# Optimization experiments

Hardware: AMD Instinct MI355X
Metric: run time of the kernel (lower is better)

## Reference

```python
import jax, jax.numpy as jnp
import numpy as np

N = 200000      # total nodes
E = 800000      # directed edges
G = 4096        # graphs in batch
D_DRUG = 128
D_CELL = 954
HID = 128
OUT = 128
EPS = 1e-5      # BatchNorm eps


def _bn(x, gamma, beta):
    # training-mode BatchNorm1d (batch statistics, biased var), dropout is eval/identity
    m = jnp.mean(x, axis=0)
    v = jnp.mean((x - m) ** 2, axis=0)
    return gamma * (x - m) * jax.lax.rsqrt(v + EPS) + beta


def _gcn_conv(x, edge_index, W, b):
    # PyG GCNConv: add self-loops, symmetric normalization, aggregate, then bias
    src = jnp.concatenate([edge_index[0], jnp.arange(N)])
    dst = jnp.concatenate([edge_index[1], jnp.arange(N)])
    ones = jnp.ones(src.shape[0], dtype=x.dtype)
    deg = jax.ops.segment_sum(ones, dst, num_segments=N)
    dinv = jnp.where(deg > 0, jax.lax.rsqrt(jnp.maximum(deg, 1.0)), 0.0)
    norm = dinv[src] * dinv[dst]                      # [E+N]
    h = x @ W                                         # [N, out]
    msg = h[src] * norm[:, None]                      # gather + scale
    out = jax.ops.segment_sum(msg, dst, num_segments=N)  # scatter-add
    return out + b


def setup_inputs() -> dict:
    key = jax.random.key(0)
    ks = jax.random.split(key, 12)
    x = jax.random.normal(ks[0], (N, D_DRUG), jnp.float32)
    edge_index = jax.random.randint(ks[1], (2, E), 0, N)
    ibatch = (jnp.arange(N) * G) // N  # sorted, every graph non-empty
    gexpr = jax.random.normal(ks[2], (G, D_CELL), jnp.float32)

    def w(k, shape):
        return jax.random.normal(k, shape, jnp.float32) / np.float32(np.sqrt(shape[0]))

    return {
        "x": x, "edge_index": edge_index, "ibatch": ibatch, "gexpr": gexpr,
        "W1": w(ks[3], (D_DRUG, HID)), "b1": jnp.zeros((HID,), jnp.float32),
        "g1": jnp.ones((HID,), jnp.float32), "be1": jnp.zeros((HID,), jnp.float32),
        "W2": w(ks[4], (HID, OUT)), "b2": jnp.zeros((OUT,), jnp.float32),
        "g2": jnp.ones((OUT,), jnp.float32), "be2": jnp.zeros((OUT,), jnp.float32),
        "Wc1": w(ks[5], (D_CELL, HID)), "bc1": jnp.zeros((HID,), jnp.float32),
        "gc": jnp.ones((HID,), jnp.float32), "bec": jnp.zeros((HID,), jnp.float32),
        "Wc2": w(ks[6], (HID, OUT)), "bc2": jnp.zeros((OUT,), jnp.float32),
    }


def reference(x, edge_index, ibatch, gexpr,
              W1, b1, g1, be1, W2, b2, g2, be2,
              Wc1, bc1, gc, bec, Wc2, bc2):
    # drug branch
    h = _gcn_conv(x, edge_index, W1, b1)
    h = _bn(jax.nn.relu(h), g1, be1)
    h = _gcn_conv(h, edge_index, W2, b2)
    h = _bn(jax.nn.relu(h), g2, be2)
    x_drug = jax.ops.segment_max(h, ibatch, num_segments=G)  # global_max_pool
    # cellline branch
    c = jnp.tanh(gexpr @ Wc1 + bc1)
    c = _bn(c, gc, bec)
    x_cell = jax.nn.relu(c @ Wc2 + bc2)
    return x_drug, x_cell
```

## Files before the change

### kernel.cpp

```cpp
#include <hip/hip_runtime.h>

#define NFEAT 128

typedef __attribute__((ext_vector_type(4))) float f32x4;
typedef __attribute__((ext_vector_type(8))) short bf16x8;

__device__ __forceinline__ unsigned short f2bf(float f) {
    unsigned u = __builtin_bit_cast(unsigned, f);
    u += 0x7fffu + ((u >> 16) & 1u);
    return (unsigned short)(u >> 16);
}
__device__ __forceinline__ float bf2f(unsigned short s) {
    unsigned u = ((unsigned)s) << 16;
    return __builtin_bit_cast(float, u);
}

__device__ __forceinline__ void dma16(const void* g, void* l) {
    __builtin_amdgcn_global_load_lds(
        (const __attribute__((address_space(1))) unsigned int*)g,
        (__attribute__((address_space(3))) unsigned int*)l, 16, 0, 0);
}

template <int ACT, typename OutT>
__device__ __forceinline__ void gemm_loop(
    int tfirst, int tstride, int tcount, int by,
    const unsigned short* __restrict__ A, const unsigned short* __restrict__ Bt,
    OutT* __restrict__ C, int M, int ldA, int ldB,
    const float* __restrict__ bias, const float* __restrict__ dscale, char* smem)
{
    unsigned short* buf0 = (unsigned short*)smem;
    unsigned short* buf1 = buf0 + 64 * 128;
    const int tid = threadIdx.x;
    const int wv = tid >> 6, lane = tid & 63;
    const int l16 = lane & 15, quad = lane >> 4;
    const int kbase = by * 128;

    const int nc0 = (wv & 1) * 64;
    bf16x8 bfr[4][4];
#pragma unroll
    for (int nt = 0; nt < 4; ++nt) {
        const unsigned short* bp =
            Bt + (size_t)(nc0 + nt * 16 + l16) * ldB + kbase + quad * 8;
#pragma unroll
        for (int ks = 0; ks < 4; ++ks)
            bfr[nt][ks] = *(const bf16x8*)(bp + ks * 32);
    }

    C += (size_t)by * M * NFEAT;
    const int rh = wv >> 1;
    const int r0 = wv * 16;

    auto stage = [&](unsigned short* dst, long tile) {
        const long t0 = tile * 64;
#pragma unroll
        for (int j = 0; j < 4; ++j) {
            const unsigned short* gp = A +
                (size_t)(t0 + r0 + j * 4 + (lane >> 4)) * ldA + kbase + l16 * 8;
            dma16(gp, (void*)&dst[(r0 + j * 4) * 128]);
        }
    };

    if (tfirst < tcount) stage(buf0, tfirst);
    __syncthreads();

    int cur = 0;
    for (long t = tfirst; t < tcount; t += tstride) {
        unsigned short* bufc = cur ? buf1 : buf0;
        unsigned short* bufn = cur ? buf0 : buf1;
        const long tn = t + tstride;
        if (tn < tcount) stage(bufn, tn);

        bf16x8 af[2][4];
#pragma unroll
        for (int mt = 0; mt < 2; ++mt) {
            const int row = rh * 32 + mt * 16 + l16;
#pragma unroll
            for (int ks = 0; ks < 4; ++ks)
                af[mt][ks] = *(const bf16x8*)(bufc + row * 128 + ks * 32 + quad * 8);
        }

        f32x4 acc[2][4];
#pragma unroll
        for (int a = 0; a < 2; ++a)
#pragma unroll
            for (int b = 0; b < 4; ++b) acc[a][b] = (f32x4){0.f, 0.f, 0.f, 0.f};
#pragma unroll
        for (int ks = 0; ks < 4; ++ks)
#pragma unroll
            for (int nt = 0; nt < 4; ++nt)
#pragma unroll
                for (int mt = 0; mt < 2; ++mt)
                    acc[mt][nt] = __builtin_amdgcn_mfma_f32_16x16x32_bf16(
                        af[mt][ks], bfr[nt][ks], acc[mt][nt], 0, 0, 0);

        const long tile0 = t * 64;
        float ds[2][4];
#pragma unroll
        for (int mt = 0; mt < 2; ++mt)
#pragma unroll
            for (int r = 0; r < 4; ++r) {
                long row = tile0 + rh * 32 + mt * 16 + quad * 4 + r;
                ds[mt][r] = dscale ? dscale[row] : 1.f;
            }
#pragma unroll
        for (int nt = 0; nt < 4; ++nt) {
            int col = nc0 + nt * 16 + l16;
            float bv = bias ? bias[col] : 0.f;
#pragma unroll
            for (int mt = 0; mt < 2; ++mt) {
                long rbase = tile0 + rh * 32 + mt * 16 + quad * 4;
#pragma unroll
                for (int r = 0; r < 4; ++r) {
                    float v = acc[mt][nt][r] + bv;
                    if (ACT == 1) v = tanhf(v);
                    if (ACT == 2) v = fmaxf(v, 0.f);
                    v *= ds[mt][r];
                    if constexpr (sizeof(OutT) == 2)
                        C[(size_t)(rbase + r) * NFEAT + col] = (OutT)f2bf(v);
                    else
                        C[(size_t)(rbase + r) * NFEAT + col] = (OutT)v;
                }
            }
        }
        __syncthreads();
        cur ^= 1;
    }
}

__global__ void k_prep(const float* __restrict__ W1, unsigned short* __restrict__ W1t,
                       const float* __restrict__ Wc1, unsigned short* __restrict__ Wc1t,
                       const float* __restrict__ gexpr, unsigned short* __restrict__ Apadh,
                       const int* __restrict__ dst, int* __restrict__ deg,
                       int G, int DC, int DCP, int E, int r1, int r2, int r3)
{
    int b = blockIdx.x, t = threadIdx.x;
    if (b < r1) {
        int idx = b * 256 + t;
        int n = idx >> 7, k = idx & 127;
        W1t[idx] = f2bf(W1[(size_t)k * NFEAT + n]);
    } else if (b < r2) {
        int idx = (b - r1) * 256 + t;
        int n = idx >> 10, k = idx & 1023;
        Wc1t[idx] = (k < DC) ? f2bf(Wc1[(size_t)k * NFEAT + n]) : (unsigned short)0;
    } else if (b < r3) {
        long idx = (long)(b - r2) * 256 + t;
        if (idx < (long)G * DCP) {
            long i = idx / DCP; int k = (int)(idx - i * DCP);
            Apadh[idx] = (k < DC) ? f2bf(gexpr[i * DC + k]) : (unsigned short)0;
        }
    } else {
        int e = (b - r3) * 256 + t;
        if (e < E) atomicAdd(&deg[dst[e]], 1);
    }
}

__device__ __forceinline__ void bnfold_body(
    int bb, const float* __restrict__ sums8, const float* __restrict__ gamma,
    const float* __restrict__ beta, float invN,
    const float* __restrict__ W, const float* __restrict__ extra,
    unsigned short* __restrict__ Wt, float* __restrict__ brow)
{
    __shared__ float ssc[128], ssh[128];
    int t = threadIdx.x;
    if (t < 128) {
        float s = 0.f, s2 = 0.f;
#pragma unroll
        for (int c = 0; c < 8; ++c) { s += sums8[c * 256 + t]; s2 += sums8[c * 256 + 128 + t]; }
        float mean = s * invN;
        float var = s2 * invN - mean * mean;
        float rstd = rsqrtf(fmaxf(var, 0.f) + 1e-5f);
        float sc = gamma[t] * rstd;
        ssc[t] = sc;
        ssh[t] = beta[t] - mean * sc;
    }
    __syncthreads();
    if (bb < 64) {
        int idx = bb * 256 + t;
        int n = idx >> 7, k = idx & 127;
        Wt[idx] = f2bf(W[(size_t)k * NFEAT + n] * ssc[k]);
    } else if (t < 128) {
        float s = extra ? extra[t] : 0.f;
        for (int k = 0; k < 128; ++k) s += ssh[k] * W[(size_t)k * NFEAT + t];
        brow[t] = s;
    }
}

__global__ void k_bnfold2(
    const float* sA, const float* gA, const float* bA, float invA,
    const float* WA, const float* eA, unsigned short* WtA, float* browA,
    const float* sB, const float* gB, const float* bB, float invB,
    const float* WB, const float* eB, unsigned short* WtB, float* browB)
{
    int b = blockIdx.x;
    if (b < 65) bnfold_body(b, sA, gA, bA, invA, WA, eA, WtA, browA);
    else        bnfold_body(b - 65, sB, gB, bB, invB, WB, eB, WtB, browB);
}

__global__ __launch_bounds__(256) void k_scan1(const int* __restrict__ deg,
        int* __restrict__ rowptr, int* __restrict__ bsum, float* __restrict__ dinv, int N)
{
    __shared__ int sh[256];
    int t = threadIdx.x;
    int base = blockIdx.x * 1024 + t * 4;
    int v[4];
#pragma unroll
    for (int j = 0; j < 4; ++j) {
        v[j] = (base + j < N) ? deg[base + j] : 0;
        if (base + j < N) dinv[base + j] = rsqrtf((float)(v[j] + 1));
    }
    int s = v[0] + v[1] + v[2] + v[3];
    sh[t] = s;
    __syncthreads();
    int incl = s;
    for (int off = 1; off < 256; off <<= 1) {
        int x = (t >= off) ? sh[t - off] : 0;
        __syncthreads();
        incl += x;
        sh[t] = incl;
        __syncthreads();
    }
    int run = incl - s;
#pragma unroll
    for (int j = 0; j < 4; ++j) {
        if (base + j < N) rowptr[base + j] = run;
        run += v[j];
    }
    if (t == 255) bsum[blockIdx.x] = incl;
}

__global__ void k_scan2(int* __restrict__ bsum, int nb)
{
    __shared__ int sh[256];
    int t = threadIdx.x;
    int s = (t < nb) ? bsum[t] : 0;
    sh[t] = s;
    __syncthreads();
    int incl = s;
    for (int off = 1; off < 256; off <<= 1) {
        int x = (t >= off) ? sh[t - off] : 0;
        __syncthreads();
        incl += x;
        sh[t] = incl;
        __syncthreads();
    }
    if (t < nb) bsum[t] = incl - s;
}

__global__ void k_scan3(int* __restrict__ rowptr, int* __restrict__ cursor,
                        const int* __restrict__ bsum, int N, int E)
{
    int i = blockIdx.x * 256 + threadIdx.x;
    if (i < N) {
        int v = rowptr[i] + bsum[i >> 10];
        rowptr[i] = v;
        cursor[i] = v;
    } else if (i == N) {
        rowptr[N] = E;
    }
}

__global__ void k_fillconv(const int* __restrict__ src, const int* __restrict__ dst,
                           int* __restrict__ cursor, int* __restrict__ csr, int E, int nf,
                           const float* __restrict__ x, unsigned short* __restrict__ xb,
                           long nfloat)
{
    const int b = blockIdx.x;
    int role, idx;
    if (b < 2 * nf) { role = b & 1; idx = b >> 1; }
    else            { role = 0;     idx = b - nf; }

    if (role == 1) {
        int e = idx * 256 + threadIdx.x;
        if (e < E) {
            int pos = atomicAdd(&cursor[dst[e]], 1);
            csr[pos] = src[e];
        }
    } else {
        long base = (long)idx * 4096 + (long)threadIdx.x * 16;
        if (base < nfloat) {
            f32x4 v0 = *(const f32x4*)(x + base);
            f32x4 v1 = *(const f32x4*)(x + base + 4);
            f32x4 v2 = *(const f32x4*)(x + base + 8);
            f32x4 v3 = *(const f32x4*)(x + base + 12);
            unsigned short o[16];
#pragma unroll
            for (int j = 0; j < 4; ++j) {
                o[j] = f2bf(v0[j]); o[4 + j] = f2bf(v1[j]);
                o[8 + j] = f2bf(v2[j]); o[12 + j] = f2bf(v3[j]);
            }
            *(uint4*)(xb + base) = *(const uint4*)&o[0];
            *(uint4*)(xb + base + 8) = *(const uint4*)&o[8];
        }
    }
}

__global__ __launch_bounds__(256) void k_pair1(
    const unsigned short* __restrict__ xb, const unsigned short* __restrict__ W1t,
    unsigned short* __restrict__ h, int N, const float* __restrict__ dinv,
    const unsigned short* __restrict__ Apadh, const unsigned short* __restrict__ Wc1t,
    float* __restrict__ pbuf, int G, int nb1, int gtiles)
{
    extern __shared__ char smem[];
    int b = blockIdx.x;
    if (b < nb1) {
        gemm_loop<0, unsigned short>(b, nb1, gtiles, 0,
                                     xb, W1t, h, N, 128, 128,
                                     nullptr, dinv, smem);
    } else {
        int cb = b - nb1;
        gemm_loop<0, float>(cb & 15, 16, 64, cb >> 4,
                            Apadh, Wc1t, pbuf, G, 1024, 1024,
                            nullptr, nullptr, smem);
    }
}

__device__ __forceinline__ void unpack_add(float* acc, uint4 a)
{
    acc[0] += bf2f((unsigned short)(a.x & 0xffff));
    acc[1] += bf2f((unsigned short)(a.x >> 16));
    acc[2] += bf2f((unsigned short)(a.y & 0xffff));
    acc[3] += bf2f((unsigned short)(a.y >> 16));
    acc[4] += bf2f((unsigned short)(a.z & 0xffff));
    acc[5] += bf2f((unsigned short)(a.z >> 16));
    acc[6] += bf2f((unsigned short)(a.w & 0xffff));
    acc[7] += bf2f((unsigned short)(a.w >> 16));
}

__device__ __forceinline__ void row_gather(const unsigned short* __restrict__ h,
    const int* __restrict__ rowptr, const int* __restrict__ csr,
    long i, int f, float* acc)
{
    int lo = rowptr[i], hi = rowptr[i + 1];
    int e = lo;
    for (; e + 3 < hi; e += 4) {
        int s0 = csr[e], s1 = csr[e + 1], s2 = csr[e + 2], s3 = csr[e + 3];
        uint4 a = *(const uint4*)(h + ((size_t)s0 << 7) + f);
        uint4 b = *(const uint4*)(h + ((size_t)s1 << 7) + f);
        uint4 c = *(const uint4*)(h + ((size_t)s2 << 7) + f);
        uint4 d = *(const uint4*)(h + ((size_t)s3 << 7) + f);
        unpack_add(acc, a); unpack_add(acc, b);
        unpack_add(acc, c); unpack_add(acc, d);
    }
    for (; e < hi; ++e) {
        int s0 = csr[e];
        uint4 a = *(const uint4*)(h + ((size_t)s0 << 7) + f);
        unpack_add(acc, a);
    }
    uint4 hs = *(const uint4*)(h + ((size_t)i << 7) + f);
    unpack_add(acc, hs);
}

__global__ __launch_bounds__(256) void k_pair2(
    const unsigned short* __restrict__ h, const int* __restrict__ rowptr,
    const int* __restrict__ csr, const float* __restrict__ dinv,
    const float* __restrict__ bias, unsigned short* __restrict__ out,
    float* __restrict__ sums8, int N, int na,
    const float* __restrict__ p, const float* __restrict__ biasC,
    unsigned short* __restrict__ cbuf, float* __restrict__ sumsC, int G)
{
    __shared__ float red[4][256];
    const int tid = threadIdx.x;
    if (blockIdx.x >= na) {
        int bb = blockIdx.x - na;
        int j = tid & 127;
        int slot = bb * 2 + (tid >> 7);
        const int nslots = 64;
        const size_t st = (size_t)G * NFEAT;
        float b = biasC[j], s = 0.f, s2 = 0.f;
        for (int i = slot; i < G; i += nslots) {
            size_t o = (size_t)i * NFEAT + j;
            float v = b;
#pragma unroll
            for (int c = 0; c < 8; ++c) v += p[o + c * st];
            v = tanhf(v);
            cbuf[o] = f2bf(v);
            s += v; s2 += v * v;
        }
        atomicAdd(&sumsC[(bb & 7) * 256 + j], s);
        atomicAdd(&sumsC[(bb & 7) * 256 + 128 + j], s2);
        return;
    }
    const int wv = tid >> 6, lane = tid & 63;
    const int f = (tid & 15) << 3;
    const long g0 = (long)blockIdx.x * 16 + (tid >> 4);
    const long gstride = (long)na * 16;

    f32x4 b0 = *(const f32x4*)&bias[f];
    f32x4 b1 = *(const f32x4*)&bias[f + 4];

    float s8[8], q8[8];
#pragma unroll
    for (int j = 0; j < 8; ++j) { s8[j] = 0.f; q8[j] = 0.f; }

    for (long i = g0; i < N; i += gstride) {
        float acc[8];
#pragma unroll
        for (int j = 0; j < 8; ++j) acc[j] = 0.f;
        row_gather(h, rowptr, csr, i, f, acc);

        float di = dinv[i];
        unsigned short o[8];
#pragma unroll
        for (int j = 0; j < 8; ++j) {
            float bj = (j < 4) ? b0[j] : b1[j - 4];
            float v = fmaxf(di * acc[j] + bj, 0.f);
            o[j] = f2bf(v);
            s8[j] += v; q8[j] += v * v;
        }
        *(uint4*)(out + (i << 7) + f) = *(const uint4*)o;
    }

#pragma unroll
    for (int j = 0; j < 8; ++j) {
        s8[j] += __shfl_xor(s8[j], 16);
        s8[j] += __shfl_xor(s8[j], 32);
        q8[j] += __shfl_xor(q8[j], 16);
        q8[j] += __shfl_xor(q8[j], 32);
    }
    if (lane < 16) {
#pragma unroll
        for (int j = 0; j < 8; ++j) {
            red[wv][f + j] = s8[j];
            red[wv][128 + f + j] = q8[j];
        }
    }
    __syncthreads();
    float tot = red[0][tid] + red[1][tid] + red[2][tid] + red[3][tid];
    atomicAdd(&sums8[(blockIdx.x & 7) * 256 + tid], tot);
}

__global__ __launch_bounds__(256) void k_pair4(
    const unsigned short* __restrict__ agg, const unsigned short* __restrict__ W2t,
    unsigned short* __restrict__ h, int N, const float* __restrict__ brow2,
    const float* __restrict__ dinv,
    const unsigned short* __restrict__ cbuf, const unsigned short* __restrict__ Wc2t,
    float* __restrict__ outc, int G, const float* __restrict__ browC,
    int nb2, int gtiles)
{
    extern __shared__ char smem[];
    int b = blockIdx.x;
    if (b < nb2) {
        gemm_loop<0, unsigned short>(b, nb2, gtiles, 0,
                                     agg, W2t, h, N, 128, 128,
                                     brow2, dinv, smem);
    } else {
        gemm_loop<2, float>(b - nb2, 64, 64, 0,
                            cbuf, Wc2t, outc, G, 128, 128,
                            browC, nullptr, smem);
    }
}

__global__ __launch_bounds__(256) void k_aggmax(
    const unsigned short* __restrict__ h, const int* __restrict__ rowptr,
    const int* __restrict__ csr, const float* __restrict__ dinv,
    const float* __restrict__ bias, int* __restrict__ gmax, int* __restrict__ gmin,
    float* __restrict__ sums8, int N, int G)
{
    __shared__ float red[4][256];
    __shared__ int lmax[288], lmin[288];
    const int tid = threadIdx.x;
    const int wv = tid >> 6, lane = tid & 63;
    const int f8 = tid & 15;
    const int f = f8 << 3;
    const int grp = tid >> 4;
    const int g_lo = blockIdx.x * 2;
    const int rstart = (int)(((long long)g_lo * N + G - 1) / G);
    const int rend   = (int)(((long long)(g_lo + 2) * N + G - 1) / G);
    const int bnd1   = (int)(((long long)(g_lo + 1) * N + G - 1) / G);

    for (int idx = tid; idx < 288; idx += 256) {
        lmax[idx] = 0;
        lmin[idx] = 0x7f800000;
    }
    __syncthreads();

    f32x4 b0 = *(const f32x4*)&bias[f];
    f32x4 b1 = *(const f32x4*)&bias[f + 4];

    float s8[8], q8[8], rmx[8], rmn[8];
#pragma unroll
    for (int j = 0; j < 8; ++j) {
        s8[j] = 0.f; q8[j] = 0.f;
        rmx[j] = 0.f; rmn[j] = __builtin_bit_cast(float, 0x7f800000);
    }
    int cur = 0;

    for (long i = rstart + grp; i < rend; i += 16) {
        float acc[8];
#pragma unroll
        for (int j = 0; j < 8; ++j) acc[j] = 0.f;
        row_gather(h, rowptr, csr, i, f, acc);

        float di = dinv[i];
        int gi = (i >= bnd1);
        if (gi != cur) {
#pragma unroll
            for (int j = 0; j < 8; ++j) {
                atomicMax(&lmax[cur * 144 + j * 16 + f8], __builtin_bit_cast(int, rmx[j]));
                atomicMin(&lmin[cur * 144 + j * 16 + f8], __builtin_bit_cast(int, rmn[j]));
                rmx[j] = 0.f; rmn[j] = __builtin_bit_cast(float, 0x7f800000);
            }
            cur = gi;
        }
#pragma unroll
        for (int j = 0; j < 8; ++j) {
            float bj = (j < 4) ? b0[j] : b1[j - 4];
            float v = fmaxf(di * acc[j] + bj, 0.f);
            s8[j] += v; q8[j] += v * v;
            rmx[j] = fmaxf(rmx[j], v);
            rmn[j] = fminf(rmn[j], v);
        }
    }
#pragma unroll
    for (int j = 0; j < 8; ++j) {
        atomicMax(&lmax[cur * 144 + j * 16 + f8], __builtin_bit_cast(int, rmx[j]));
        atomicMin(&lmin[cur * 144 + j * 16 + f8], __builtin_bit_cast(int, rmn[j]));
    }

#pragma unroll
    for (int j = 0; j < 8; ++j) {
        s8[j] += __shfl_xor(s8[j], 16);
        s8[j] += __shfl_xor(s8[j], 32);
        q8[j] += __shfl_xor(q8[j], 16);
        q8[j] += __shfl_xor(q8[j], 32);
    }
    if (lane < 16) {
#pragma unroll
        for (int j = 0; j < 8; ++j) {
            red[wv][f + j] = s8[j];
            red[wv][128 + f + j] = q8[j];
        }
    }
    __syncthreads();
    float tot = red[0][tid] + red[1][tid] + red[2][tid] + red[3][tid];
    atomicAdd(&sums8[(blockIdx.x & 7) * 256 + tid], tot);

    for (int idx = tid; idx < 2 * 128; idx += 256) {
        int gg = idx >> 7, feat = idx & 127;
        int a = gg * 144 + (feat & 7) * 16 + (feat >> 3);
        gmax[(size_t)(g_lo + gg) * 128 + feat] = lmax[a];
        gmin[(size_t)(g_lo + gg) * 128 + feat] = lmin[a];
    }
}

__global__ void k_segfin(const float* __restrict__ sums8, const float* __restrict__ gamma,
                         const float* __restrict__ beta, const int* __restrict__ gmax,
                         const int* __restrict__ gmin, float* __restrict__ out,
                         float invN, int total)
{
    __shared__ float ssc[128], ssh[128];
    int t = threadIdx.x;
    if (t < 128) {
        float s = 0.f, s2 = 0.f;
#pragma unroll
        for (int c = 0; c < 8; ++c) { s += sums8[c * 256 + t]; s2 += sums8[c * 256 + 128 + t]; }
        float mean = s * invN;
        float var = s2 * invN - mean * mean;
        float rstd = rsqrtf(fmaxf(var, 0.f) + 1e-5f);
        float sc = gamma[t] * rstd;
        ssc[t] = sc;
        ssh[t] = beta[t] - mean * sc;
    }
    __syncthreads();
    int idx = blockIdx.x * 256 + t;
    if (idx < total) {
        int j = idx & 127;
        float sc = ssc[j], sh = ssh[j];
        int bits = (sc >= 0.f) ? gmax[idx] : gmin[idx];
        out[idx] = sc * __builtin_bit_cast(float, bits) + sh;
    }
}

extern "C" void kernel_launch(void* const* d_in, const int* in_sizes, int n_in,
                              void* d_out, int out_size, void* d_ws, size_t ws_size,
                              hipStream_t stream)
{
    const float* x     = (const float*)d_in[0];
    const int*   ei    = (const int*)d_in[1];
    const float* gexpr = (const float*)d_in[3];
    const float* W1  = (const float*)d_in[4];
    const float* b1  = (const float*)d_in[5];
    const float* g1  = (const float*)d_in[6];
    const float* be1 = (const float*)d_in[7];
    const float* W2  = (const float*)d_in[8];
    const float* b2  = (const float*)d_in[9];
    const float* g2  = (const float*)d_in[10];
    const float* be2 = (const float*)d_in[11];
    const float* Wc1 = (const float*)d_in[12];
    const float* bc1 = (const float*)d_in[13];
    const float* gc  = (const float*)d_in[14];
    const float* bec = (const float*)d_in[15];
    const float* Wc2 = (const float*)d_in[16];
    const float* bc2 = (const float*)d_in[17];

    const int N = in_sizes[0] / NFEAT;
    const int E = in_sizes[1] / 2;
    const int G = in_sizes[3] / 954;
    const int DC = 954, DCP = 1024;

    char* wsp = (char*)d_ws;
    size_t off = 0;
    auto alloc = [&](size_t bytes) -> char* {
        char* p = wsp + off;
        off += (bytes + 255) & ~(size_t)255;
        return p;
    };
    unsigned short* agg    = (unsigned short*)alloc((size_t)N * NFEAT * 2);
    unsigned short* h      = (unsigned short*)alloc((size_t)N * NFEAT * 2);
    unsigned short* xb     = (unsigned short*)alloc((size_t)N * NFEAT * 2);
    float*          dinv   = (float*)alloc((size_t)N * 4);
    int*            deg    = (int*)alloc((size_t)N * 4);
    int*            rowptr = (int*)alloc((size_t)(N + 1) * 4);
    int*            cursor = (int*)alloc((size_t)N * 4);
    int*            csr    = (int*)alloc((size_t)E * 4);
    int*            bsum   = (int*)alloc(256 * 4);
    unsigned short* Apadh  = (unsigned short*)alloc((size_t)G * DCP * 2);
    float*          pbuf   = (float*)alloc((size_t)8 * G * NFEAT * 4);
    unsigned short* cbuf   = (unsigned short*)alloc((size_t)G * NFEAT * 2);
    int*            gmax   = (int*)alloc((size_t)G * NFEAT * 4);
    int*            gmin   = (int*)alloc((size_t)G * NFEAT * 4);
    unsigned short* W1t    = (unsigned short*)alloc(128 * 128 * 2);
    unsigned short* W2t    = (unsigned short*)alloc(128 * 128 * 2);
    unsigned short* Wc1t   = (unsigned short*)alloc(128 * DCP * 2);
    unsigned short* Wc2t   = (unsigned short*)alloc(128 * 128 * 2);
    float*          stats  = (float*)alloc(8192 * 4);
    float* sums1 = stats,         * sums2 = stats + 2048, * sumsC = stats + 4096;
    float* brow2  = stats + 6400, * browC  = stats + 6528;

    hipMemsetAsync(stats, 0, 6144 * 4, stream);
    hipMemsetAsync(deg, 0, (size_t)N * 4, stream);

    const int* esrc = ei;
    const int* edst = ei + E;

    const int r1 = 64;
    const int r2 = r1 + 512;
    const int r3 = r2 + (int)(((long)G * DCP + 255) / 256);
    const int rtot = r3 + (E + 255) / 256;
    k_prep<<<rtot, 256, 0, stream>>>(W1, W1t, Wc1, Wc1t, gexpr, Apadh,
                                     edst, deg, G, DC, DCP, E, r1, r2, r3);

    const int nb = (N + 1023) / 1024;
    k_scan1<<<nb, 256, 0, stream>>>(deg, rowptr, bsum, dinv, N);
    k_scan2<<<1, 256, 0, stream>>>(bsum, nb);
    k_scan3<<<(N + 1 + 255) / 256, 256, 0, stream>>>(rowptr, cursor, bsum, N, E);

    const int gtiles = N / 64;
    const int nf = (E + 255) / 256;
    const long nfloat = (long)N * NFEAT;
    const int nconv = (int)((nfloat + 4095) / 4096);
    const int ablocks = 2048;
    const int NB1 = 1024;
    const int NB2 = 768;

    k_fillconv<<<nf + nconv, 256, 0, stream>>>(
        esrc, edst, cursor, csr, E, nf, x, xb, nfloat);

    k_pair1<<<NB1 + 128, 256, 2 * 64 * 128 * 2, stream>>>(
        xb, W1t, h, N, dinv,
        Apadh, Wc1t, pbuf, G, NB1, gtiles);

    k_pair2<<<ablocks + 32, 256, 0, stream>>>(
        h, rowptr, csr, dinv, b1, agg, sums1, N, ablocks,
        pbuf, bc1, cbuf, sumsC, G);

    k_bnfold2<<<130, 256, 0, stream>>>(
        sums1, g1, be1, 1.f / (float)N, W2, nullptr, W2t, brow2,
        sumsC, gc, bec, 1.f / (float)G, Wc2, bc2, Wc2t, browC);

    float* outp = (float*)d_out;
    k_pair4<<<NB2 + 64, 256, 2 * 64 * 128 * 2, stream>>>(
        agg, W2t, h, N, brow2, dinv,
        cbuf, Wc2t, outp + (size_t)G * NFEAT, G, browC, NB2, gtiles);

    k_aggmax<<<G / 2, 256, 0, stream>>>(h, rowptr, csr, dinv, b2, gmax, gmin, sums2, N, G);

    k_segfin<<<(G * NFEAT + 255) / 256, 256, 0, stream>>>(
        sums2, g2, be2, gmax, gmin, outp, 1.f / (float)N, G * NFEAT);
}
```

Before: 441.3 us.

## Fuse cell-line GEMM split-K reduction with tanh and BN stats into one pass

The cell-line first layer used to run as a split-K GEMM that wrote 8 float partial buffers, which a separate part of the aggregation kernel then summed, passed through tanh and reduced into BN statistics. Now each of 64 blocks computes a full 64-row tile over all K=1024 with a double-buffered MFMA loop, then applies bias and tanh, writes bf16, and accumulates BN sums with wave shuffles plus atomics. This removes the 16 MB partial-buffer round trip and the extra reduction blocks. In exchange the cell branch has less parallelism: fewer blocks, each with a long serial K loop.

```diff
diff --git a/kernel.cpp b/kernel.cpp
--- a/kernel.cpp
+++ b/kernel.cpp
@@ -124,6 +124,109 @@
         }
         __syncthreads();
         cur ^= 1;
+    }
+}
+
+__device__ __forceinline__ void cell1_loop(
+    int bx, int slot, const unsigned short* __restrict__ Apadh,
+    const unsigned short* __restrict__ Wc1t, unsigned short* __restrict__ cbuf,
+    const float* __restrict__ bc1, float* __restrict__ sumsC, char* smem)
+{
+    unsigned short* buf0 = (unsigned short*)smem;
+    unsigned short* buf1 = buf0 + 64 * 128;
+    const long tile0 = (long)bx * 64;
+    const int tid = threadIdx.x;
+    const int wv = tid >> 6, lane = tid & 63;
+    const int l16 = lane & 15, quad = lane >> 4;
+    const int nc0 = (wv & 1) * 64;
+    const int rh = wv >> 1;
+    const int r0 = wv * 16;
+
+    auto stage = [&](unsigned short* dst, int w) {
+#pragma unroll
+        for (int j = 0; j < 4; ++j) {
+            const unsigned short* gp = Apadh +
+                (size_t)(tile0 + r0 + j * 4 + (lane >> 4)) * 1024 + w * 128 + l16 * 8;
+            dma16(gp, (void*)&dst[(r0 + j * 4) * 128]);
+        }
+    };
+
+    f32x4 acc[2][4];
+#pragma unroll
+    for (int a = 0; a < 2; ++a)
+#pragma unroll
+        for (int b = 0; b < 4; ++b) acc[a][b] = (f32x4){0.f, 0.f, 0.f, 0.f};
+
+    stage(buf0, 0);
+    __syncthreads();
+
+    int cur = 0;
+    for (int w = 0; w < 8; ++w) {
+        unsigned short* bufc = cur ? buf1 : buf0;
+        unsigned short* bufn = cur ? buf0 : buf1;
+        if (w + 1 < 8) stage(bufn, w + 1);
+
+        bf16x8 bfr[4][4];
+#pragma unroll
+        for (int nt = 0; nt < 4; ++nt) {
+            const unsigned short* bp =
+                Wc1t + (size_t)(nc0 + nt * 16 + l16) * 1024 + w * 128 + quad * 8;
+#pragma unroll
+            for (int ks = 0; ks < 4; ++ks)
+                bfr[nt][ks] = *(const bf16x8*)(bp + ks * 32);
+        }
+
+        bf16x8 af[2][4];
+#pragma unroll
+        for (int mt = 0; mt < 2; ++mt) {
+            const int row = rh * 32 + mt * 16 + l16;
+#pragma unroll
+            for (int ks = 0; ks < 4; ++ks)
+                af[mt][ks] = *(const bf16x8*)(bufc + row * 128 + ks * 32 + quad * 8);
+        }
+#pragma unroll
+        for (int ks = 0; ks < 4; ++ks)
+#pragma unroll
+            for (int nt = 0; nt < 4; ++nt)
+#pragma unroll
+                for (int mt = 0; mt < 2; ++mt)
+                    acc[mt][nt] = __builtin_amdgcn_mfma_f32_16x16x32_bf16(
+                        af[mt][ks], bfr[nt][ks], acc[mt][nt], 0, 0, 0);
+
+        __syncthreads();
+        cur ^= 1;
+    }
+
+    float s[4], q[4];
+#pragma unroll
+    for (int nt = 0; nt < 4; ++nt) { s[nt] = 0.f; q[nt] = 0.f; }
+#pragma unroll
+    for (int nt = 0; nt < 4; ++nt) {
+        int col = nc0 + nt * 16 + l16;
+        float bv = bc1[col];
+#pragma unroll
+        for (int mt = 0; mt < 2; ++mt) {
+            long rbase = tile0 + rh * 32 + mt * 16 + quad * 4;
+#pragma unroll
+            for (int r = 0; r < 4; ++r) {
+                float v = tanhf(acc[mt][nt][r] + bv);
+                cbuf[(size_t)(rbase + r) * NFEAT + col] = f2bf(v);
+                s[nt] += v; q[nt] += v * v;
+            }
+        }
+    }
+#pragma unroll
+    for (int nt = 0; nt < 4; ++nt) {
+        s[nt] += __shfl_xor(s[nt], 16); s[nt] += __shfl_xor(s[nt], 32);
+        q[nt] += __shfl_xor(q[nt], 16); q[nt] += __shfl_xor(q[nt], 32);
+    }
+    if (quad == 0) {
+#pragma unroll
+        for (int nt = 0; nt < 4; ++nt) {
+            int col = nc0 + nt * 16 + l16;
+            atomicAdd(&sumsC[slot * 256 + col], s[nt]);
+            atomicAdd(&sumsC[slot * 256 + 128 + col], q[nt]);
+        }
     }
 }
 
@@ -298,7 +401,8 @@
     const unsigned short* __restrict__ xb, const unsigned short* __restrict__ W1t,
     unsigned short* __restrict__ h, int N, const float* __restrict__ dinv,
     const unsigned short* __restrict__ Apadh, const unsigned short* __restrict__ Wc1t,
-    float* __restrict__ pbuf, int G, int nb1, int gtiles)
+    unsigned short* __restrict__ cbuf, const float* __restrict__ bc1,
+    float* __restrict__ sumsC, int nb1, int gtiles)
 {
     extern __shared__ char smem[];
     int b = blockIdx.x;
@@ -308,9 +412,7 @@
                                      nullptr, dinv, smem);
     } else {
         int cb = b - nb1;
-        gemm_loop<0, float>(cb & 15, 16, 64, cb >> 4,
-                            Apadh, Wc1t, pbuf, G, 1024, 1024,
-                            nullptr, nullptr, smem);
+        cell1_loop(cb, cb & 7, Apadh, Wc1t, cbuf, bc1, sumsC, smem);
     }
 }
 
@@ -350,40 +452,18 @@
     unpack_add(acc, hs);
 }
 
-__global__ __launch_bounds__(256) void k_pair2(
+__global__ __launch_bounds__(256) void k_agg(
     const unsigned short* __restrict__ h, const int* __restrict__ rowptr,
     const int* __restrict__ csr, const float* __restrict__ dinv,
     const float* __restrict__ bias, unsigned short* __restrict__ out,
-    float* __restrict__ sums8, int N, int na,
-    const float* __restrict__ p, const float* __restrict__ biasC,
-    unsigned short* __restrict__ cbuf, float* __restrict__ sumsC, int G)
+    float* __restrict__ sums8, int N)
 {
     __shared__ float red[4][256];
     const int tid = threadIdx.x;
-    if (blockIdx.x >= na) {
-        int bb = blockIdx.x - na;
-        int j = tid & 127;
-        int slot = bb * 2 + (tid >> 7);
-        const int nslots = 64;
-        const size_t st = (size_t)G * NFEAT;
-        float b = biasC[j], s = 0.f, s2 = 0.f;
-        for (int i = slot; i < G; i += nslots) {
-            size_t o = (size_t)i * NFEAT + j;
-            float v = b;
-#pragma unroll
-            for (int c = 0; c < 8; ++c) v += p[o + c * st];
-            v = tanhf(v);
-            cbuf[o] = f2bf(v);
-            s += v; s2 += v * v;
-        }
-        atomicAdd(&sumsC[(bb & 7) * 256 + j], s);
-        atomicAdd(&sumsC[(bb & 7) * 256 + 128 + j], s2);
-        return;
-    }
     const int wv = tid >> 6, lane = tid & 63;
     const int f = (tid & 15) << 3;
     const long g0 = (long)blockIdx.x * 16 + (tid >> 4);
-    const long gstride = (long)na * 16;
+    const long gstride = (long)gridDim.x * 16;
 
     f32x4 b0 = *(const f32x4*)&bias[f];
     f32x4 b1 = *(const f32x4*)&bias[f + 4];
@@ -615,7 +695,6 @@
     int*            csr    = (int*)alloc((size_t)E * 4);
     int*            bsum   = (int*)alloc(256 * 4);
     unsigned short* Apadh  = (unsigned short*)alloc((size_t)G * DCP * 2);
-    float*          pbuf   = (float*)alloc((size_t)8 * G * NFEAT * 4);
     unsigned short* cbuf   = (unsigned short*)alloc((size_t)G * NFEAT * 2);
     int*            gmax   = (int*)alloc((size_t)G * NFEAT * 4);
     int*            gmin   = (int*)alloc((size_t)G * NFEAT * 4);
@@ -656,13 +735,11 @@
     k_fillconv<<<nf + nconv, 256, 0, stream>>>(
         esrc, edst, cursor, csr, E, nf, x, xb, nfloat);
 
-    k_pair1<<<NB1 + 128, 256, 2 * 64 * 128 * 2, stream>>>(
+    k_pair1<<<NB1 + G / 64, 256, 2 * 64 * 128 * 2, stream>>>(
         xb, W1t, h, N, dinv,
-        Apadh, Wc1t, pbuf, G, NB1, gtiles);
-
-    k_pair2<<<ablocks + 32, 256, 0, stream>>>(
-        h, rowptr, csr, dinv, b1, agg, sums1, N, ablocks,
-        pbuf, bc1, cbuf, sumsC, G);
+        Apadh, Wc1t, cbuf, bc1, sumsC, NB1, gtiles);
+
+    k_agg<<<ablocks, 256, 0, stream>>>(h, rowptr, csr, dinv, b1, agg, sums1, N);
 
     k_bnfold2<<<130, 256, 0, stream>>>(
         sums1, g1, be1, 1.f / (float)N, W2, nullptr, W2t, brow2,
```

After: 453.2 us. 2.7% more time.
